# Kernel tuning notes

Hardware: AMD Instinct MI355X
Metric: run time of the kernel (lower is better)

## Reference

```python
import jax, jax.numpy as jnp
import numpy as np


def conv1x1(x, w, b):
    # x: [B,C,H,W], w: [O,C], b: [O]
    return jnp.einsum('bchw,oc->bohw', x, w) + b[None, :, None, None]


def conv3x3(x, w, b):
    # x: [B,C,H,W], w: [O,C,3,3]
    y = jax.lax.conv_general_dilated(
        x, w, window_strides=(1, 1), padding='SAME',
        dimension_numbers=('NCHW', 'OIHW', 'NCHW'))
    return y + b[None, :, None, None]


def setup_inputs() -> dict:
    key = jax.random.key(0)
    ks = jax.random.split(key, 20)

    def u(k, shape, fan_in):
        # PyTorch Conv2d default init: uniform(-1/sqrt(fan_in), 1/sqrt(fan_in))
        s = 1.0 / np.sqrt(fan_in)
        return jax.random.uniform(k, shape, jnp.float32, -s, s)

    B, H, W = 4, 64, 64
    return {
        'x':   jax.random.normal(ks[0], (B, 3, H, W), jnp.float32),
        # 1x1 stem convs (weights stored as [O,C])
        'w1':  u(ks[1], (64, 3), 3),        'b1':  u(ks[2], (64,), 3),
        'w2':  u(ks[3], (128, 64), 64),     'b2':  u(ks[4], (128,), 64),
        'w3':  u(ks[5], (256, 128), 128),   'b3':  u(ks[6], (256,), 128),
        # 3x3 conv branch (fan_in = 256*9)
        'wb1': u(ks[7], (256, 256, 3, 3), 256 * 9), 'bb1': u(ks[8], (256,), 256 * 9),
        'wb2': u(ks[9], (256, 256, 3, 3), 256 * 9), 'bb2': u(ks[10], (256,), 256 * 9),
        # q/k/v 1x1 convs
        'wq':  u(ks[11], (256, 256), 256),  'bq':  u(ks[12], (256,), 256),
        'wk':  u(ks[13], (256, 256), 256),  'bk':  u(ks[14], (256,), 256),
        'wv':  u(ks[15], (256, 256), 256),  'bv':  u(ks[16], (256,), 256),
        'alpha': jnp.float32(0.5),
        'beta':  jnp.float32(0.5),
    }


def reference(x, w1, b1, w2, b2, w3, b3, wb1, bb1, wb2, bb2,
              wq, bq, wk, bk, wv, bv, alpha, beta):
    x = jax.nn.relu(conv1x1(x, w1, b1))
    x = jax.nn.relu(conv1x1(x, w2, b2))
    x = jax.nn.relu(conv1x1(x, w3, b3))          # [B,256,H,W]
    conv_out = conv3x3(jax.nn.relu(conv3x3(x, wb1, bb1)), wb2, bb2)
    B, C, H, W = x.shape
    q = conv1x1(x, wq, bq).reshape(B, C, -1)     # [B,C,N]
    k = conv1x1(x, wk, bk).reshape(B, C, -1)     # [B,C,N]
    v = conv1x1(x, wv, bv).reshape(B, C, -1)     # [B,C,N]
    # torch: bmm(k^T, q) -> [B,N,N], softmax over last dim
    attn = jax.nn.softmax(jnp.einsum('bcn,bcm->bnm', k, q), axis=-1)
    # torch: bmm(v, attn) -> [B,C,N]
    attn_out = jnp.einsum('bcn,bnm->bcm', v, attn).reshape(B, C, H, W)
    return alpha * conv_out + beta * attn_out
```

## Files before the change

kernel.cpp:

```cpp
#include <hip/hip_runtime.h>
#include <math.h>

#define NPIX 4096
#define CC   256

typedef __attribute__((ext_vector_type(8))) short bf16x8;
typedef __attribute__((ext_vector_type(4))) float f32x4;

__device__ inline unsigned short f2bf(float f) {
    unsigned u = __builtin_bit_cast(unsigned, f);
    u += 0x7FFF + ((u >> 16) & 1);
    return (unsigned short)(u >> 16);
}
__device__ inline float bf2f(unsigned short h) {
    unsigned u = (unsigned)h << 16;
    return __builtin_bit_cast(float, u);
}
__device__ inline void gl_lds16(const void* g, void* l) {
    __builtin_amdgcn_global_load_lds(
        (const __attribute__((address_space(1))) void*)g,
        (__attribute__((address_space(3))) void*)l, 16, 0, 0);
}

__global__ __launch_bounds__(256) void prep_kernel(
    const float* __restrict__ w2, const float* __restrict__ w3,
    const float* __restrict__ wq, const float* __restrict__ wk,
    const float* __restrict__ wv, const float* __restrict__ wb1,
    const float* __restrict__ wb2, const float* __restrict__ bq,
    const float* __restrict__ bk,
    unsigned short* w2b, unsigned short* w3b, unsigned short* wqb,
    unsigned short* wkb, unsigned short* wvb,
    unsigned short* wr1, unsigned short* wr2, float* bqk) {
    int i = blockIdx.x * 256 + threadIdx.x;
    if (i < 8192)  w2b[i] = f2bf(w2[i]);
    if (i < 32768) w3b[i] = f2bf(w3[i]);
    if (i < 65536) { wqb[i] = f2bf(wq[i]); wkb[i] = f2bf(wk[i]); wvb[i] = f2bf(wv[i]); }
    if (i < 256)   { bqk[i] = bq[i]; bqk[256 + i] = bk[i]; }
    if (i < 589824) {
        int o = i / 2304; int r = i - o * 2304; int tap = r >> 8; int c = r & 255;
        wr1[i] = f2bf(wb1[(o * 256 + c) * 9 + tap]);
        wr2[i] = f2bf(wb2[(o * 256 + c) * 9 + tap]);
    }
}

__global__ __launch_bounds__(256) void stem1_kernel(
    const float* __restrict__ x, const float* __restrict__ w1,
    const float* __restrict__ b1, unsigned short* __restrict__ h1T) {
    int idx = blockIdx.x * 256 + threadIdx.x;
    int o = idx & 63;
    int p = (idx >> 6) & 4095;
    int b = idx >> 18;
    const float* xb = x + (size_t)b * 3 * NPIX + p;
    float acc = b1[o];
    acc = fmaf(w1[o * 3 + 0], xb[0],        acc);
    acc = fmaf(w1[o * 3 + 1], xb[NPIX],     acc);
    acc = fmaf(w1[o * 3 + 2], xb[2 * NPIX], acc);
    h1T[idx] = f2bf(fmaxf(acc, 0.f));
}

template<int EPI, int KK>
__global__ __launch_bounds__(256) void gemm_fullk(
    const unsigned short* __restrict__ A, long lda, long sA,
    const unsigned short* __restrict__ BT, long ldb, long sB,
    void* __restrict__ Cp, long ldc, long sC,
    const float* __restrict__ bias, float* __restrict__ aux) {
    constexpr int SPR = KK / 8;
    constexpr int RPI = 64 / SPR;
    __shared__ unsigned short As[128 * KK];
    __shared__ unsigned short Bs[128 * KK];
    const int tid  = threadIdx.x;
    const int lane = tid & 63;
    const int wave = tid >> 6;
    const int wr = (wave >> 1) * 64, wc = (wave & 1) * 64;
    const int l15 = lane & 15, lh = lane >> 4;
    const int sl  = lane & (SPR - 1);
    const int rof = lane / SPR;
    const int z = blockIdx.z;
    const unsigned short* Ab = A  + (size_t)z * sA + (size_t)blockIdx.y * 128 * lda;
    const unsigned short* Bb = BT + (size_t)z * sB + (size_t)blockIdx.x * 128 * ldb;

    f32x4 acc[4][4];
    #pragma unroll
    for (int i = 0; i < 4; ++i)
        #pragma unroll
        for (int j = 0; j < 4; ++j) { f32x4 zr = {0.f, 0.f, 0.f, 0.f}; acc[i][j] = zr; }

    #pragma unroll
    for (int i = 0; i < KK / 16; ++i) {
        int r0  = wave * 32 + i * RPI;
        int row = r0 + rof;
        int cs  = (sl ^ (row & (SPR - 1))) * 8;
        gl_lds16(Ab + (size_t)row * lda + cs, &As[r0 * KK]);
        gl_lds16(Bb + (size_t)row * ldb + cs, &Bs[r0 * KK]);
    }
    __syncthreads();

    #pragma unroll
    for (int ks = 0; ks < KK / 32; ++ks) {
        bf16x8 a[4], b[4];
        #pragma unroll
        for (int f = 0; f < 4; ++f) {
            int ra = wr + f * 16 + l15;
            a[f] = *(const bf16x8*)&As[ra * KK + ((((ks << 2) + lh) ^ (ra & (SPR - 1))) << 3)];
            int rb = wc + f * 16 + l15;
            b[f] = *(const bf16x8*)&Bs[rb * KK + ((((ks << 2) + lh) ^ (rb & (SPR - 1))) << 3)];
        }
        #pragma unroll
        for (int i = 0; i < 4; ++i)
            #pragma unroll
            for (int j = 0; j < 4; ++j)
                acc[i][j] = __builtin_amdgcn_mfma_f32_16x16x32_bf16(
                    a[i], b[j], acc[i][j], 0, 0, 0);
    }

    const int row0 = blockIdx.y * 128 + wr;
    const int col0 = blockIdx.x * 128 + wc;
    unsigned short* OUT = (unsigned short*)Cp + (size_t)z * sC;
    #pragma unroll
    for (int i = 0; i < 4; ++i)
        #pragma unroll
        for (int j = 0; j < 4; ++j) {
            int cgl = col0 + j * 16 + l15;
            float bc = (EPI == 1 || EPI == 2) ? bias[cgl] : 0.f;
            float sc = (EPI == 3) ? aux[(size_t)z * 4096 + cgl] : 1.f;
            #pragma unroll
            for (int q = 0; q < 4; ++q) {
                int r = row0 + i * 16 + lh * 4 + q;
                float v = acc[i][j][q];
                if (EPI == 3) v = (v + bias[r]) * sc;
                else v += bc;
                if (EPI == 1) v = fmaxf(v, 0.f);
                OUT[(size_t)r * ldc + cgl] = f2bf(v);
            }
        }
}

template<int EPI>
__global__ __launch_bounds__(256) void gemm128(
    const unsigned short* __restrict__ A, long lda, long sA,
    const unsigned short* __restrict__ BT, long ldb, long sB,
    int Kc, int splits, int nb,
    void* __restrict__ Cp, long ldc, long sC,
    float* __restrict__ aux, unsigned short* __restrict__ partial,
    const unsigned short* __restrict__ CV,
    const float* __restrict__ alphaP, const float* __restrict__ betaP,
    int nwgc) {
    __shared__ unsigned short As[2][128 * 64];
    __shared__ unsigned short Bs[2][128 * 64];
    const int orig = blockIdx.x;
    const int wgid = (orig & 7) * nwgc + (orig >> 3);
    int bx, by, sp, z;
    if (EPI == 0) {
        bx = wgid & 31; by = (wgid >> 5) & 31; z = wgid >> 10; sp = 0;
    } else {
        bx = wgid & 31; by = (wgid >> 5) & 1;
        sp = (wgid >> 6) % splits; z = wgid / (64 * splits);
    }

    const int tid  = threadIdx.x;
    const int lane = tid & 63;
    const int wave = tid >> 6;
    const int wr = (wave >> 1) * 64, wc = (wave & 1) * 64;
    const int l15 = lane & 15, lh = lane >> 4;
    const int sl  = lane & 7, rof = lane >> 3;
    const unsigned short* Ab = A  + (size_t)z * sA + (size_t)by * 128 * lda + (size_t)sp * Kc;
    const unsigned short* Bb = BT + (size_t)z * sB + (size_t)bx * 128 * ldb + (size_t)sp * Kc;

    f32x4 acc[4][4];
    #pragma unroll
    for (int i = 0; i < 4; ++i)
        #pragma unroll
        for (int j = 0; j < 4; ++j) { f32x4 zr = {0.f, 0.f, 0.f, 0.f}; acc[i][j] = zr; }

    auto STAGE = [&](int buf, int k0) {
        #pragma unroll
        for (int s = 0; s < 4; ++s) {
            int rb  = wave * 8 + s * 32;
            int row = rb + rof;
            int cs  = (sl ^ (row & 7)) * 8;
            gl_lds16(Ab + (size_t)row * lda + k0 + cs, &As[buf][rb * 64]);
            gl_lds16(Bb + (size_t)row * ldb + k0 + cs, &Bs[buf][rb * 64]);
        }
    };

    STAGE(0, 0);
    const int T = Kc >> 6;
    for (int t = 0; t < T; ++t) {
        const int cur = t & 1;
        if (t + 1 < T) {
            STAGE(cur ^ 1, (t + 1) << 6);
            asm volatile("s_waitcnt vmcnt(8)" ::: "memory");
        } else {
            asm volatile("s_waitcnt vmcnt(0)" ::: "memory");
        }
        __builtin_amdgcn_s_barrier();
        asm volatile("" ::: "memory");
        __builtin_amdgcn_s_setprio(1);
        #pragma unroll
        for (int ks = 0; ks < 2; ++ks) {
            bf16x8 a[4], b[4];
            #pragma unroll
            for (int f = 0; f < 4; ++f) {
                int ra = wr + f * 16 + l15;
                a[f] = *(const bf16x8*)&As[cur][ra * 64 + ((((ks << 2) + lh) ^ (ra & 7)) << 3)];
                int rb = wc + f * 16 + l15;
                b[f] = *(const bf16x8*)&Bs[cur][rb * 64 + ((((ks << 2) + lh) ^ (rb & 7)) << 3)];
            }
            #pragma unroll
            for (int i = 0; i < 4; ++i)
                #pragma unroll
                for (int j = 0; j < 4; ++j)
                    acc[i][j] = __builtin_amdgcn_mfma_f32_16x16x32_bf16(
                        a[i], b[j], acc[i][j], 0, 0, 0);
        }
        __builtin_amdgcn_s_setprio(0);
        asm volatile("" ::: "memory");
        __builtin_amdgcn_s_barrier();
    }

    if (EPI == 0) {
        unsigned short* OUT = (unsigned short*)Cp + (size_t)z * sC;
        const int row0 = by * 128 + wr;
        const int col0 = bx * 128 + wc;
        float cs4[4] = {0.f, 0.f, 0.f, 0.f};
        #pragma unroll
        for (int i = 0; i < 4; ++i)
            #pragma unroll
            for (int j = 0; j < 4; ++j) {
                int cgl = col0 + j * 16 + l15;
                #pragma unroll
                for (int q = 0; q < 4; ++q) {
                    int r = row0 + i * 16 + lh * 4 + q;
                    unsigned short h = f2bf(__expf(acc[i][j][q]));
                    OUT[(size_t)r * ldc + cgl] = h;
                    cs4[j] += bf2f(h);
                }
            }
        #pragma unroll
        for (int off = 16; off <= 32; off <<= 1)
            #pragma unroll
            for (int j = 0; j < 4; ++j)
                cs4[j] += __shfl_xor(cs4[j], off);
        if (lh == 0) {
            float* part = aux + (((size_t)z * 32 + by) * 2 + (wave >> 1)) * 4096;
            #pragma unroll
            for (int j = 0; j < 4; ++j)
                part[col0 + j * 16 + l15] = cs4[j];
        }
    } else {
        const int col0 = bx * 128 + wc;
        const int row0 = by * 128 + wr;
        if (splits == 1) {
            float* OUT = (float*)Cp + (size_t)z * sC;
            const unsigned short* CVb = CV + (size_t)z * sC;
            const float al = alphaP[0], be = betaP[0];
            #pragma unroll
            for (int i = 0; i < 4; ++i)
                #pragma unroll
                for (int j = 0; j < 4; ++j) {
                    int cgl = col0 + j * 16 + l15;
                    #pragma unroll
                    for (int q = 0; q < 4; ++q) {
                        int r = row0 + i * 16 + lh * 4 + q;
                        size_t o = (size_t)r * ldc + cgl;
                        OUT[o] = al * bf2f(CVb[o]) + be * acc[i][j][q];
                    }
                }
        } else {
            unsigned short* P = partial + ((size_t)sp * nb + z) * ((size_t)256 * 4096);
            #pragma unroll
            for (int i = 0; i < 4; ++i)
                #pragma unroll
                for (int j = 0; j < 4; ++j) {
                    int cgl = col0 + j * 16 + l15;
                    #pragma unroll
                    for (int q = 0; q < 4; ++q) {
                        int r = row0 + i * 16 + lh * 4 + q;
                        P[(size_t)r * 4096 + cgl] = f2bf(acc[i][j][q]);
                    }
                }
        }
    }
}

__global__ __launch_bounds__(256) void reduce_kernel(
    const unsigned short* __restrict__ partial, const unsigned short* __restrict__ cvb,
    const float* __restrict__ alphaP, const float* __restrict__ betaP,
    float* __restrict__ outp, int splits, long chunk) {
    long idx = ((long)blockIdx.x * 256 + threadIdx.x) * 4;
    if (idx >= chunk) return;
    float s0 = 0.f, s1 = 0.f, s2 = 0.f, s3 = 0.f;
    for (int sp = 0; sp < splits; ++sp) {
        ushort4 p = *(const ushort4*)&partial[(size_t)sp * chunk + idx];
        s0 += bf2f(p.x); s1 += bf2f(p.y); s2 += bf2f(p.z); s3 += bf2f(p.w);
    }
    ushort4 c4 = *(const ushort4*)&cvb[idx];
    const float al = alphaP[0], be = betaP[0];
    float4 r;
    r.x = al * bf2f(c4.x) + be * s0;
    r.y = al * bf2f(c4.y) + be * s1;
    r.z = al * bf2f(c4.z) + be * s2;
    r.w = al * bf2f(c4.w) + be * s3;
    *(float4*)&outp[idx] = r;
}

__global__ __launch_bounds__(256) void recip_kernel(
    const float* __restrict__ part, float* __restrict__ rcp) {
    int idx = blockIdx.x * 256 + threadIdx.x;
    int z = idx >> 12, n = idx & 4095;
    const float* pb = part + (size_t)z * 64 * 4096 + n;
    float s = 0.f;
    #pragma unroll 8
    for (int t = 0; t < 64; ++t) s += pb[(size_t)t * 4096];
    rcp[idx] = 1.f / s;
}

template<int PIXOUT>
__global__ __launch_bounds__(256) void conv3_v3(
    const unsigned short* __restrict__ X, const unsigned short* __restrict__ Wr,
    const float* __restrict__ bias, void* __restrict__ Outp) {
    __shared__ unsigned short wt[9 * 64 * 40];
    __shared__ unsigned short patch[264 * 40];
    const int tid  = threadIdx.x;
    const int lane = tid & 63;
    const int wave = tid >> 6;
    const int l15 = lane & 15, lh = lane >> 4;
    const int ob = blockIdx.x & 3;
    const int b  = blockIdx.x >> 2;
    const int h0 = blockIdx.y;
    const int obase = (wave & 1) * 32;
    const int pbase = (wave >> 1) * 64;
    const unsigned short* Xb  = X + (size_t)b * (NPIX * CC);
    const unsigned short* Wro = Wr + (size_t)ob * 64 * 2304;

    constexpr int NI = PIXOUT ? 4 : 2;
    constexpr int NJ = PIXOUT ? 2 : 4;
    f32x4 acc[NI][NJ];
    #pragma unroll
    for (int i = 0; i < NI; ++i)
        #pragma unroll
        for (int j = 0; j < NJ; ++j) { f32x4 zr = {0.f, 0.f, 0.f, 0.f}; acc[i][j] = zr; }

    for (int c0 = 0; c0 < 256; c0 += 32) {
        __syncthreads();
        #pragma unroll
        for (int t = 0; t < 5; ++t) {
            int q = t * 256 + tid;
            if (q < 1056) {
                int slot = q >> 2, cg = (q & 3) * 8;
                int r = slot / 66, w = slot - r * 66;
                int hh = h0 * 2 - 1 + r, ww = w - 1;
                int4 v = make_int4(0, 0, 0, 0);
                if ((unsigned)hh < 64u && (unsigned)ww < 64u)
                    v = *(const int4*)&Xb[(size_t)(hh * 64 + ww) * 256 + c0 + cg];
                *(int4*)&patch[slot * 40 + cg] = v;
            }
        }
        #pragma unroll
        for (int t = 0; t < 9; ++t) {
            int q = t * 256 + tid;
            int o = q / 36, rem = q - o * 36;
            int tap = rem >> 2, cg = (rem & 3) * 8;
            int4 v = *(const int4*)&Wro[(size_t)o * 2304 + tap * 256 + c0 + cg];
            *(int4*)&wt[(tap * 64 + o) * 40 + cg] = v;
        }
        __syncthreads();
        #pragma unroll
        for (int tap = 0; tap < 9; ++tap) {
            const int dy = tap / 3 - 1, dx = tap % 3 - 1;
            bf16x8 wf[2], pf[4];
            #pragma unroll
            for (int f = 0; f < 2; ++f) {
                int o = obase + f * 16 + l15;
                wf[f] = *(const bf16x8*)&wt[(tap * 64 + o) * 40 + lh * 8];
            }
            #pragma unroll
            for (int f = 0; f < 4; ++f) {
                int p = pbase + f * 16 + l15;
                int slot = ((p >> 6) + dy + 1) * 66 + (p & 63) + dx + 1;
                pf[f] = *(const bf16x8*)&patch[slot * 40 + lh * 8];
            }
            if (PIXOUT) {
                #pragma unroll
                for (int i = 0; i < NI; ++i)
                    #pragma unroll
                    for (int j = 0; j < NJ; ++j)
                        acc[i][j] = __builtin_amdgcn_mfma_f32_16x16x32_bf16(
                            pf[i], wf[j], acc[i][j], 0, 0, 0);
            } else {
                #pragma unroll
                for (int i = 0; i < NI; ++i)
                    #pragma unroll
                    for (int j = 0; j < NJ; ++j)
                        acc[i][j] = __builtin_amdgcn_mfma_f32_16x16x32_bf16(
                            wf[i], pf[j], acc[i][j], 0, 0, 0);
            }
        }
    }

    const int P0 = h0 * 128;
    if (PIXOUT) {
        unsigned short* O = (unsigned short*)Outp + (size_t)b * (NPIX * CC);
        #pragma unroll
        for (int i = 0; i < 4; ++i)
            #pragma unroll
            for (int j = 0; j < 2; ++j) {
                int o = ob * 64 + obase + j * 16 + l15;
                float bb = bias[o];
                #pragma unroll
                for (int q = 0; q < 4; ++q) {
                    int p = pbase + i * 16 + lh * 4 + q;
                    float v = fmaxf(acc[i][j][q] + bb, 0.f);
                    O[(size_t)(P0 + p) * CC + o] = f2bf(v);
                }
            }
    } else {
        unsigned short* O = (unsigned short*)Outp + (size_t)b * (CC * NPIX);
        #pragma unroll
        for (int i = 0; i < 2; ++i)
            #pragma unroll
            for (int j = 0; j < 4; ++j) {
                #pragma unroll
                for (int q = 0; q < 4; ++q) {
                    int o = ob * 64 + obase + i * 16 + lh * 4 + q;
                    int p = pbase + j * 16 + l15;
                    O[(size_t)o * NPIX + P0 + p] = f2bf(acc[i][j][q] + bias[o]);
                }
            }
    }
}

extern "C" void kernel_launch(void* const* d_in, const int* in_sizes, int n_in,
                              void* d_out, int out_size, void* d_ws, size_t ws_size,
                              hipStream_t stream) {
    const float* x   = (const float*)d_in[0];
    const float* w1  = (const float*)d_in[1];  const float* b1  = (const float*)d_in[2];
    const float* w2  = (const float*)d_in[3];  const float* b2  = (const float*)d_in[4];
    const float* w3  = (const float*)d_in[5];  const float* b3  = (const float*)d_in[6];
    const float* wb1 = (const float*)d_in[7];  const float* bb1 = (const float*)d_in[8];
    const float* wb2 = (const float*)d_in[9];  const float* bb2 = (const float*)d_in[10];
    const float* wq  = (const float*)d_in[11]; const float* bq  = (const float*)d_in[12];
    const float* wk  = (const float*)d_in[13]; const float* bk  = (const float*)d_in[14];
    const float* wv  = (const float*)d_in[15]; const float* bv  = (const float*)d_in[16];
    const float* alpha = (const float*)d_in[17];
    const float* beta  = (const float*)d_in[18];

    const size_t MB = 1 << 20;
    char* wsb = (char*)d_ws;
    unsigned short* x3T = (unsigned short*)(wsb + 0 * MB);
    unsigned short* qkT = (unsigned short*)(wsb + 8 * MB);
    unsigned short* cv  = (unsigned short*)(wsb + 24 * MB);
    unsigned short* t1T = (unsigned short*)(wsb + 32 * MB);
    unsigned short* h1T = (unsigned short*)(wsb + 32 * MB);
    unsigned short* h2T = (unsigned short*)(wsb + 34 * MB);
    unsigned short* vB  = (unsigned short*)(wsb + 40 * MB);
    unsigned short* w2b = (unsigned short*)(wsb + 48 * MB);
    unsigned short* w3b = w2b + 8192;
    unsigned short* wqb = w3b + 32768;
    unsigned short* wkb = wqb + 65536;
    unsigned short* wvb = wkb + 65536;
    unsigned short* wr1 = wvb + 65536;
    unsigned short* wr2 = wr1 + 589824;
    float*          bqk  = (float*)(wsb + 51 * MB);
    float*          part = (float*)(wsb + 52 * MB);
    float*          rcp  = (float*)(wsb + 56 * MB);
    unsigned short* ST   = (unsigned short*)(wsb + 57 * MB);
    float* out = (float*)d_out;
    const long ONEM = (long)CC * NPIX;
    const long SS = 4096L * 4096;

    int nb, splits;
    if      (ws_size >= (size_t)249 * MB) { nb = 4; splits = 8;  }
    else if (ws_size >= (size_t)185 * MB) { nb = 2; splits = 16; }
    else if (ws_size >= (size_t)121 * MB) { nb = 1; splits = 16; }
    else                                  { nb = 1; splits = 1;  }
    unsigned short* pvpart = (unsigned short*)(wsb + (size_t)(57 + nb * 32) * MB);

    prep_kernel<<<2304, 256, 0, stream>>>(w2, w3, wq, wk, wv, wb1, wb2, bq, bk,
                                          w2b, w3b, wqb, wkb, wvb, wr1, wr2, bqk);
    stem1_kernel<<<4096, 256, 0, stream>>>(x, w1, b1, h1T);

    gemm_fullk<1, 64><<<dim3(1, 32, 4), 256, 0, stream>>>(
        h1T, 64, 4096L * 64, w2b, 64, 0,
        h2T, 128, 4096L * 128, b2, nullptr);
    gemm_fullk<1, 128><<<dim3(2, 32, 4), 256, 0, stream>>>(
        h2T, 128, 4096L * 128, w3b, 128, 0,
        x3T, 256, 4096L * 256, b3, nullptr);
    gemm_fullk<2, 256><<<dim3(4, 32, 4), 256, 0, stream>>>(
        x3T, 256, 4096L * 256, wqb, 256, 0,
        qkT, 512, 4096L * 512, bqk, nullptr);
    conv3_v3<1><<<dim3(16, 32), 256, 0, stream>>>(x3T, wr1, bb1, t1T);
    conv3_v3<0><<<dim3(16, 32), 256, 0, stream>>>(t1T, wr2, bb2, cv);

    for (int b0 = 0; b0 < 4; b0 += nb) {
        int nwgS = 1024 * nb;
        gemm128<0><<<nwgS, 256, 0, stream>>>(
            qkT + (size_t)b0 * 4096 * 512, 512, 4096L * 512,
            qkT + (size_t)b0 * 4096 * 512 + 256, 512, 4096L * 512,
            256, 1, nb, ST, 4096, SS,
            part, nullptr, nullptr, nullptr, nullptr, nwgS / 8);
        recip_kernel<<<nb * 16, 256, 0, stream>>>(part, rcp);
        gemm_fullk<3, 256><<<dim3(32, 2, nb), 256, 0, stream>>>(
            wvb, 256, 0,
            x3T + (size_t)b0 * 4096 * 256, 256, 4096L * 256,
            vB, 4096, 256L * 4096, bv, rcp);
        int nwgP = 64 * splits * nb;
        gemm128<4><<<nwgP, 256, 0, stream>>>(
            vB, 4096, 256L * 4096, ST, 4096, SS,
            4096 / splits, splits, nb,
            out + (size_t)b0 * ONEM, 4096, ONEM,
            nullptr, pvpart, cv + (size_t)b0 * ONEM, alpha, beta, nwgP / 8);
        if (splits > 1)
            reduce_kernel<<<nb * 1024, 256, 0, stream>>>(
                pvpart, cv + (size_t)b0 * ONEM, alpha, beta,
                out + (size_t)b0 * ONEM, splits, (long)nb * ONEM);
    }
}
```

Baseline: 240.3 us.

## Drop split-K PV reduction and load conv3 weights directly to LDS

Removes split-K from the attention PV GEMM so each workgroup covers the full K range and writes the alpha/beta-combined output directly, eliminating bf16 partial buffers and the separate reduce kernel. The conv3x3 kernel now streams its weight tile with global_load_lds into an unpadded LDS layout instead of register-staged copies. Tradeoff: far fewer workgroups in the PV GEMM (less parallelism, longer serial K loop), and the unpadded weight layout may cause LDS bank conflicts.

```diff
diff --git a/kernel.cpp b/kernel.cpp
--- a/kernel.cpp
+++ b/kernel.cpp
@@ -250,58 +250,22 @@
     } else {
         const int col0 = bx * 128 + wc;
         const int row0 = by * 128 + wr;
-        if (splits == 1) {
-            float* OUT = (float*)Cp + (size_t)z * sC;
-            const unsigned short* CVb = CV + (size_t)z * sC;
-            const float al = alphaP[0], be = betaP[0];
-            #pragma unroll
-            for (int i = 0; i < 4; ++i)
-                #pragma unroll
-                for (int j = 0; j < 4; ++j) {
-                    int cgl = col0 + j * 16 + l15;
-                    #pragma unroll
-                    for (int q = 0; q < 4; ++q) {
-                        int r = row0 + i * 16 + lh * 4 + q;
-                        size_t o = (size_t)r * ldc + cgl;
-                        OUT[o] = al * bf2f(CVb[o]) + be * acc[i][j][q];
-                    }
+        float* OUT = (float*)Cp + (size_t)z * sC;
+        const unsigned short* CVb = CV + (size_t)z * sC;
+        const float al = alphaP[0], be = betaP[0];
+        #pragma unroll
+        for (int i = 0; i < 4; ++i)
+            #pragma unroll
+            for (int j = 0; j < 4; ++j) {
+                int cgl = col0 + j * 16 + l15;
+                #pragma unroll
+                for (int q = 0; q < 4; ++q) {
+                    int r = row0 + i * 16 + lh * 4 + q;
+                    size_t o = (size_t)r * ldc + cgl;
+                    OUT[o] = al * bf2f(CVb[o]) + be * acc[i][j][q];
                 }
-        } else {
-            unsigned short* P = partial + ((size_t)sp * nb + z) * ((size_t)256 * 4096);
-            #pragma unroll
-            for (int i = 0; i < 4; ++i)
-                #pragma unroll
-                for (int j = 0; j < 4; ++j) {
-                    int cgl = col0 + j * 16 + l15;
-                    #pragma unroll
-                    for (int q = 0; q < 4; ++q) {
-                        int r = row0 + i * 16 + lh * 4 + q;
-                        P[(size_t)r * 4096 + cgl] = f2bf(acc[i][j][q]);
-                    }
-                }
-        }
-    }
-}
-
-__global__ __launch_bounds__(256) void reduce_kernel(
-    const unsigned short* __restrict__ partial, const unsigned short* __restrict__ cvb,
-    const float* __restrict__ alphaP, const float* __restrict__ betaP,
-    float* __restrict__ outp, int splits, long chunk) {
-    long idx = ((long)blockIdx.x * 256 + threadIdx.x) * 4;
-    if (idx >= chunk) return;
-    float s0 = 0.f, s1 = 0.f, s2 = 0.f, s3 = 0.f;
-    for (int sp = 0; sp < splits; ++sp) {
-        ushort4 p = *(const ushort4*)&partial[(size_t)sp * chunk + idx];
-        s0 += bf2f(p.x); s1 += bf2f(p.y); s2 += bf2f(p.z); s3 += bf2f(p.w);
-    }
-    ushort4 c4 = *(const ushort4*)&cvb[idx];
-    const float al = alphaP[0], be = betaP[0];
-    float4 r;
-    r.x = al * bf2f(c4.x) + be * s0;
-    r.y = al * bf2f(c4.y) + be * s1;
-    r.z = al * bf2f(c4.z) + be * s2;
-    r.w = al * bf2f(c4.w) + be * s3;
-    *(float4*)&outp[idx] = r;
+            }
+    }
 }
 
 __global__ __launch_bounds__(256) void recip_kernel(
@@ -316,10 +280,10 @@
 }
 
 template<int PIXOUT>
-__global__ __launch_bounds__(256) void conv3_v3(
+__global__ __launch_bounds__(256) void conv3_v4(
     const unsigned short* __restrict__ X, const unsigned short* __restrict__ Wr,
     const float* __restrict__ bias, void* __restrict__ Outp) {
-    __shared__ unsigned short wt[9 * 64 * 40];
+    __shared__ unsigned short wt[9 * 64 * 32];
     __shared__ unsigned short patch[264 * 40];
     const int tid  = threadIdx.x;
     const int lane = tid & 63;
@@ -332,6 +296,7 @@
     const int pbase = (wave >> 1) * 64;
     const unsigned short* Xb  = X + (size_t)b * (NPIX * CC);
     const unsigned short* Wro = Wr + (size_t)ob * 64 * 2304;
+    const size_t wgbase = (size_t)(wave * 16 + (lane >> 2)) * 2304 + (lane & 3) * 8;
 
     constexpr int NI = PIXOUT ? 4 : 2;
     constexpr int NJ = PIXOUT ? 2 : 4;
@@ -343,6 +308,9 @@
 
     for (int c0 = 0; c0 < 256; c0 += 32) {
         __syncthreads();
+        #pragma unroll
+        for (int s = 0; s < 9; ++s)
+            gl_lds16(Wro + wgbase + s * 256 + c0, &wt[(s * 64 + wave * 16) * 32]);
         #pragma unroll
         for (int t = 0; t < 5; ++t) {
             int q = t * 256 + tid;
@@ -356,14 +324,6 @@
                 *(int4*)&patch[slot * 40 + cg] = v;
             }
         }
-        #pragma unroll
-        for (int t = 0; t < 9; ++t) {
-            int q = t * 256 + tid;
-            int o = q / 36, rem = q - o * 36;
-            int tap = rem >> 2, cg = (rem & 3) * 8;
-            int4 v = *(const int4*)&Wro[(size_t)o * 2304 + tap * 256 + c0 + cg];
-            *(int4*)&wt[(tap * 64 + o) * 40 + cg] = v;
-        }
         __syncthreads();
         #pragma unroll
         for (int tap = 0; tap < 9; ++tap) {
@@ -372,7 +332,7 @@
             #pragma unroll
             for (int f = 0; f < 2; ++f) {
                 int o = obase + f * 16 + l15;
-                wf[f] = *(const bf16x8*)&wt[(tap * 64 + o) * 40 + lh * 8];
+                wf[f] = *(const bf16x8*)&wt[(tap * 64 + o) * 32 + lh * 8];
             }
             #pragma unroll
             for (int f = 0; f < 4; ++f) {
@@ -469,12 +429,10 @@
     const long ONEM = (long)CC * NPIX;
     const long SS = 4096L * 4096;
 
-    int nb, splits;
-    if      (ws_size >= (size_t)249 * MB) { nb = 4; splits = 8;  }
-    else if (ws_size >= (size_t)185 * MB) { nb = 2; splits = 16; }
-    else if (ws_size >= (size_t)121 * MB) { nb = 1; splits = 16; }
-    else                                  { nb = 1; splits = 1;  }
-    unsigned short* pvpart = (unsigned short*)(wsb + (size_t)(57 + nb * 32) * MB);
+    int nb;
+    if      (ws_size >= (size_t)185 * MB) nb = 4;
+    else if (ws_size >= (size_t)121 * MB) nb = 2;
+    else                                  nb = 1;
 
     prep_kernel<<<2304, 256, 0, stream>>>(w2, w3, wq, wk, wv, wb1, wb2, bq, bk,
                                           w2b, w3b, wqb, wkb, wvb, wr1, wr2, bqk);
@@ -489,8 +447,8 @@
     gemm_fullk<2, 256><<<dim3(4, 32, 4), 256, 0, stream>>>(
         x3T, 256, 4096L * 256, wqb, 256, 0,
         qkT, 512, 4096L * 512, bqk, nullptr);
-    conv3_v3<1><<<dim3(16, 32), 256, 0, stream>>>(x3T, wr1, bb1, t1T);
-    conv3_v3<0><<<dim3(16, 32), 256, 0, stream>>>(t1T, wr2, bb2, cv);
+    conv3_v4<1><<<dim3(16, 32), 256, 0, stream>>>(x3T, wr1, bb1, t1T);
+    conv3_v4<0><<<dim3(16, 32), 256, 0, stream>>>(t1T, wr2, bb2, cv);
 
     for (int b0 = 0; b0 < 4; b0 += nb) {
         int nwgS = 1024 * nb;
@@ -504,15 +462,11 @@
             wvb, 256, 0,
             x3T + (size_t)b0 * 4096 * 256, 256, 4096L * 256,
             vB, 4096, 256L * 4096, bv, rcp);
-        int nwgP = 64 * splits * nb;
+        int nwgP = 64 * nb;
         gemm128<4><<<nwgP, 256, 0, stream>>>(
             vB, 4096, 256L * 4096, ST, 4096, SS,
-            4096 / splits, splits, nb,
+            4096, 1, nb,
             out + (size_t)b0 * ONEM, 4096, ONEM,
-            nullptr, pvpart, cv + (size_t)b0 * ONEM, alpha, beta, nwgP / 8);
-        if (splits > 1)
-            reduce_kernel<<<nb * 1024, 256, 0, stream>>>(
-                pvpart, cv + (size_t)b0 * ONEM, alpha, beta,
-                out + (size_t)b0 * ONEM, splits, (long)nb * ONEM);
-    }
-}
+            nullptr, nullptr, cv + (size_t)b0 * ONEM, alpha, beta, nwgP / 8);
+    }
+}
```

Result: no change. 239.0 us (-0.5%).
